# Performance work log

Measured on AMD Instinct MI355X. Metric: run time of the kernel, lower is better.

## Reference

```python
import jax, jax.numpy as jnp
import numpy as np

B, L, D = 4, 2048, 1024
H = 16
HD = D // H


def setup_inputs() -> dict:
    key = jax.random.key(0)
    ks = jax.random.split(key, 6)
    x = jax.random.normal(ks[0], (B, L, D), dtype=jnp.float32)
    # True = masked-out (strict upper triangle -> causal)
    causal_mask = jnp.triu(jnp.ones((L, L), dtype=bool), k=1)
    key_padding_mask = jnp.zeros((B, L), dtype=bool)  # no padding
    lim = 1.0 / np.sqrt(D)
    Wqkv = jax.random.uniform(ks[1], (3 * D, D), minval=-lim, maxval=lim, dtype=jnp.float32)
    bqkv = jax.random.uniform(ks[2], (3 * D,), minval=-lim, maxval=lim, dtype=jnp.float32)
    Wproj = jax.random.uniform(ks[3], (D, D), minval=-lim, maxval=lim, dtype=jnp.float32)
    bproj = jax.random.uniform(ks[4], (D,), minval=-lim, maxval=lim, dtype=jnp.float32)
    return {"x": x, "causal_mask": causal_mask, "key_padding_mask": key_padding_mask,
            "Wqkv": Wqkv, "bqkv": bqkv, "Wproj": Wproj, "bproj": bproj}


def reference(x, causal_mask, key_padding_mask, Wqkv, bqkv, Wproj, bproj):
    b, l, d = x.shape
    scale = (d // H // 1) ** 0  # placeholder; real scale below
    scale = (d // H) ** -0.5
    qkv = x @ Wqkv.T + bqkv                      # [B,L,3D]
    qkv = qkv.reshape(b, l, 3, H, HD).transpose(2, 0, 3, 1, 4)  # [3,B,H,L,HD]
    q, k, v = qkv[0], qkv[1], qkv[2]
    attn = jnp.einsum('bhqd,bhkd->bhqk', q, k) * scale          # [B,H,L,L]
    neg_inf = jnp.float32(-jnp.inf)
    attn = jnp.where(causal_mask[None, None, :, :], neg_inf, attn)
    attn = jnp.where(key_padding_mask[:, None, None, :], neg_inf, attn)
    attn = jax.nn.softmax(attn, axis=-1)
    attn = jnp.nan_to_num(attn, nan=0.0, posinf=0.0, neginf=0.0)
    out = jnp.einsum('bhqk,bhkd->bhqd', attn, v)                # [B,H,L,HD]
    out = out.transpose(0, 2, 1, 3).reshape(b, l, d)
    return out @ Wproj.T + bproj
```

## Files before the change

kernel.cpp:

```cpp
#include <hip/hip_runtime.h>

typedef __bf16 bf16;
typedef __attribute__((ext_vector_type(8))) __bf16 bf16x8;
typedef __attribute__((ext_vector_type(4))) __bf16 bf16x4;
typedef __attribute__((ext_vector_type(4))) float f32x4;
typedef __attribute__((ext_vector_type(4))) short short4v;

#define AS1C(p) ((const __attribute__((address_space(1))) void*)(p))
#define AS3(p)  ((__attribute__((address_space(3))) void*)(p))

static __device__ __forceinline__ f32x4 pv_mfma(bf16x4 a, bf16x4 b, f32x4 c) {
#if __has_builtin(__builtin_amdgcn_mfma_f32_16x16x16bf16_1k)
  return __builtin_amdgcn_mfma_f32_16x16x16bf16_1k(
      __builtin_bit_cast(short4v, a), __builtin_bit_cast(short4v, b), c, 0, 0, 0);
#else
  f32x4 d = c;
  asm("v_mfma_f32_16x16x16_bf16 %0, %1, %2, %0" : "+v"(d) : "v"(a), "v"(b));
  return d;
#endif
}

static __device__ __forceinline__ float fexp2(float x) {
#if __has_builtin(__builtin_amdgcn_exp2f)
  return __builtin_amdgcn_exp2f(x);
#else
  return exp2f(x);
#endif
}
static __device__ __forceinline__ float m3(float a, float b, float c) {
  return fmaxf(fmaxf(a, b), c);
}

__global__ void castk(const float* __restrict__ in, bf16* __restrict__ out, long n) {
  long i = ((long)blockIdx.x * blockDim.x + threadIdx.x) * 4;
  if (i >= n) return;
  f32x4 v = *reinterpret_cast<const f32x4*>(in + i);
  bf16x4 o;
  o[0] = (bf16)v[0]; o[1] = (bf16)v[1]; o[2] = (bf16)v[2]; o[3] = (bf16)v[3];
  *reinterpret_cast<bf16x4*>(out + i) = o;
}

template<int MODE>
__global__ __launch_bounds__(256, 2)
void gemm_bt(const bf16* __restrict__ A, const bf16* __restrict__ BT,
             const float* __restrict__ bias, void* __restrict__ Cout,
             int M, int N, int K) {
  __shared__ bf16 As[128 * 64];
  __shared__ bf16 Bs[128 * 64];
  const int tid = threadIdx.x;
  const int lane = tid & 63;
  const int w = tid >> 6;
  const int wm = w >> 1, wn = w & 1;
  const int row0 = blockIdx.y * 128, col0 = blockIdx.x * 128;

  f32x4 acc[4][4] = {};

  const int srow = tid >> 3;
  const int scb = ((tid & 7) << 4) ^ ((srow & 7) << 4);
  const long aoff = (long)(row0 + srow) * K + (scb >> 1);
  const long boff = (long)(col0 + srow) * K + (scb >> 1);

  for (int k0 = 0; k0 < K; k0 += 64) {
    #pragma unroll
    for (int i = 0; i < 4; ++i) {
      __builtin_amdgcn_global_load_lds(AS1C(A + aoff + (long)i * 32 * K + k0),
                                       AS3((char*)As + i * 4096 + w * 1024), 16, 0, 0);
      __builtin_amdgcn_global_load_lds(AS1C(BT + boff + (long)i * 32 * K + k0),
                                       AS3((char*)Bs + i * 4096 + w * 1024), 16, 0, 0);
    }
    __syncthreads();
    #pragma unroll
    for (int kf = 0; kf < 2; ++kf) {
      bf16x8 af[4], bfr[4];
      #pragma unroll
      for (int m = 0; m < 4; ++m) {
        int r = wm * 64 + m * 16 + (lane & 15);
        int cb = (kf * 64 + ((lane >> 4) << 4)) ^ ((r & 7) << 4);
        af[m] = *reinterpret_cast<const bf16x8*>((const char*)As + r * 128 + cb);
      }
      #pragma unroll
      for (int n = 0; n < 4; ++n) {
        int r = wn * 64 + n * 16 + (lane & 15);
        int cb = (kf * 64 + ((lane >> 4) << 4)) ^ ((r & 7) << 4);
        bfr[n] = *reinterpret_cast<const bf16x8*>((const char*)Bs + r * 128 + cb);
      }
      #pragma unroll
      for (int m = 0; m < 4; ++m)
        #pragma unroll
        for (int n = 0; n < 4; ++n) {
          if constexpr (MODE == 1)
            acc[m][n] = __builtin_amdgcn_mfma_f32_16x16x32_bf16(bfr[n], af[m], acc[m][n], 0, 0, 0);
          else
            acc[m][n] = __builtin_amdgcn_mfma_f32_16x16x32_bf16(af[m], bfr[n], acc[m][n], 0, 0, 0);
        }
    }
    __syncthreads();
  }

  const int g = lane >> 4, q = lane & 15;

  if constexpr (MODE == 0) {
    #pragma unroll
    for (int m = 0; m < 4; ++m)
      #pragma unroll
      for (int n = 0; n < 4; ++n)
        #pragma unroll
        for (int r = 0; r < 4; ++r) {
          int grow = row0 + wm * 64 + m * 16 + g * 4 + r;
          int gcol = col0 + wn * 64 + n * 16 + q;
          reinterpret_cast<float*>(Cout)[(long)grow * N + gcol] = acc[m][n][r] + bias[gcol];
        }
  } else if constexpr (MODE == 1) {
    const int t = (int)blockIdx.x >> 3;
    const int h = (((int)blockIdx.x << 1) | wn) & 15;
    const float qs = (t == 0) ? 0.125f * 1.44269504f : 1.0f;
    bf16* outb = reinterpret_cast<bf16*>(Cout) + (t ? 8388608 : 0);
    #pragma unroll
    for (int n = 0; n < 4; ++n) {
      f32x4 bv = *reinterpret_cast<const f32x4*>(bias + col0 + wn * 64 + n * 16 + g * 4);
      #pragma unroll
      for (int m = 0; m < 4; ++m) {
        int grow = row0 + wm * 64 + m * 16 + q;
        int bb = grow >> 11, ll = grow & 2047;
        bf16x4 o;
        #pragma unroll
        for (int r = 0; r < 4; ++r) o[r] = (bf16)((acc[m][n][r] + bv[r]) * qs);
        *reinterpret_cast<bf16x4*>(outb + ((long)(bb * 16 + h) * 2048 + ll) * 64 + n * 16 + g * 4) = o;
      }
    }
  } else {
    const int h = (((int)blockIdx.x << 1) | wn) & 15;
    bf16* outb = reinterpret_cast<bf16*>(Cout);
    #pragma unroll
    for (int n = 0; n < 4; ++n) {
      float bv = bias[col0 + wn * 64 + n * 16 + q];
      int hd = n * 16 + q;
      #pragma unroll
      for (int m = 0; m < 4; ++m) {
        int grow = row0 + wm * 64 + m * 16 + g * 4;
        int bb = grow >> 11, ll = grow & 2047;
        bf16x4 o;
        #pragma unroll
        for (int r = 0; r < 4; ++r) o[r] = (bf16)(acc[m][n][r] + bv);
        *reinterpret_cast<bf16x4*>(outb + ((long)(bb * 16 + h) * 64 + hd) * 2048 + ll) = o;
      }
    }
  }
}

__global__ __launch_bounds__(512, 8)
void attn_fwd(const bf16* __restrict__ Qg, const bf16* __restrict__ Kg,
              const bf16* __restrict__ VTg, bf16* __restrict__ Og) {
  __shared__ bf16 Ks[2][64 * 64];
  __shared__ bf16 Vs[2][64 * 64];
  const int tid = threadIdx.x, lane = tid & 63, w = tid >> 6;
  const int g = lane >> 4, q = lane & 15;

  const int orig = blockIdx.x;
  const int wgid = (orig & 7) * 128 + (orig >> 3);
  const int bh = wgid >> 4;
  const int qi = 15 - (wgid & 15);
  const int bb = bh >> 4, h = bh & 15;
  const long base = (long)bh * (2048 * 64);
  const int q0 = qi * 128;
  const int qw = q0 + w * 16;
  const int myq = qw + q;

  bf16x8 qf[2];
  qf[0] = *reinterpret_cast<const bf16x8*>(Qg + base + (long)myq * 64 + g * 8);
  qf[1] = *reinterpret_cast<const bf16x8*>(Qg + base + (long)myq * 64 + 32 + g * 8);

  f32x4 accO[4] = {};
  float m = -1e30f, l = 0.f;

  const int srow = tid >> 3;
  const int scb = ((tid & 7) << 4) ^ ((srow & 7) << 4);
  const int nt = 2 * qi + 2;
  const int ntw = (qw >> 6) + 1;

  auto stage = [&](int kt, int buf) {
    __builtin_amdgcn_global_load_lds(
        AS1C(Kg + base + (long)(kt * 64 + srow) * 64 + (scb >> 1)),
        AS3((char*)&Ks[buf][0] + tid * 16), 16, 0, 0);
    __builtin_amdgcn_global_load_lds(
        AS1C(VTg + base + (long)srow * 2048 + kt * 64 + (scb >> 1)),
        AS3((char*)&Vs[buf][0] + tid * 16), 16, 0, 0);
  };

  stage(0, 0);

  for (int kt = 0; kt < nt; ++kt) {
    const int cur = kt & 1;
    __syncthreads();
    if (kt + 1 < nt) stage(kt + 1, cur ^ 1);
    if (kt >= ntw) continue;

    const char* Kb = (const char*)&Ks[cur][0];
    const char* Vb = (const char*)&Vs[cur][0];

    f32x4 sT[4] = {};
    __builtin_amdgcn_s_setprio(1);
    #pragma unroll
    for (int kf = 0; kf < 2; ++kf)
      #pragma unroll
      for (int a = 0; a < 4; ++a) {
        int r = a * 16 + q;
        int cb = (kf * 64 + g * 16) ^ ((r & 7) << 4);
        bf16x8 kb = *reinterpret_cast<const bf16x8*>(Kb + r * 128 + cb);
        sT[a] = __builtin_amdgcn_mfma_f32_16x16x32_bf16(kb, qf[kf], sT[a], 0, 0, 0);
      }
    __builtin_amdgcn_s_setprio(0);

    if (kt == ntw - 1) {
      #pragma unroll
      for (int a = 0; a < 4; ++a)
        #pragma unroll
        for (int r = 0; r < 4; ++r) {
          int kv = kt * 64 + a * 16 + 4 * g + r;
          if (kv > myq) sT[a][r] = -1e30f;
        }
    }

    {
      float t0 = m3(sT[0][0], sT[0][1], sT[0][2]);
      float t1 = m3(sT[0][3], sT[1][0], sT[1][1]);
      float t2 = m3(sT[1][2], sT[1][3], sT[2][0]);
      float t3 = m3(sT[2][1], sT[2][2], sT[2][3]);
      float t4 = m3(sT[3][0], sT[3][1], sT[3][2]);
      float vm = fmaxf(m3(t0, t1, t2), m3(t3, t4, sT[3][3]));
      vm = fmaxf(vm, __shfl_xor(vm, 16));
      vm = fmaxf(vm, __shfl_xor(vm, 32));
      if (__ballot(vm > m + 8.0f)) {
        float mnew = fmaxf(m, vm);
        float fac = fexp2(m - mnew);
        m = mnew;
        #pragma unroll
        for (int b = 0; b < 4; ++b) accO[b] *= fac;
        l *= fac;
      }
    }
    float ps = 0.f;
    bf16x4 pa[4];
    #pragma unroll
    for (int a = 0; a < 4; ++a)
      #pragma unroll
      for (int r = 0; r < 4; ++r) {
        float p = fexp2(sT[a][r] - m);
        ps += p;
        pa[a][r] = (bf16)p;
      }
    ps += __shfl_xor(ps, 16);
    ps += __shfl_xor(ps, 32);
    l += ps;

    __builtin_amdgcn_s_setprio(1);
    #pragma unroll
    for (int a = 0; a < 4; ++a)
      #pragma unroll
      for (int b = 0; b < 4; ++b) {
        int row = b * 16 + q;
        int cb = (a * 32 + g * 8) ^ ((row & 7) << 4);
        bf16x4 vfrag = *reinterpret_cast<const bf16x4*>(Vb + row * 128 + cb);
        accO[b] = pv_mfma(vfrag, pa[a], accO[b]);
      }
    __builtin_amdgcn_s_setprio(0);
  }

  __syncthreads();
  char* ob = (char*)&Ks[0][0] + w * 2048;
  float rl = 1.0f / l;
  #pragma unroll
  for (int b = 0; b < 4; ++b)
    #pragma unroll
    for (int r = 0; r < 4; ++r) {
      int hd = 16 * b + 4 * g + r;
      int cb = (hd * 2) ^ ((q & 7) << 4);
      *reinterpret_cast<bf16*>(ob + q * 128 + cb) = (bf16)(accO[b][r] * rl);
    }
  asm volatile("s_waitcnt lgkmcnt(0)" ::: "memory");
  __builtin_amdgcn_sched_barrier(0);

  const int rr = lane >> 2, cc = lane & 3;
  #pragma unroll
  for (int half = 0; half < 2; ++half) {
    int hd0 = cc * 16 + half * 8;
    int cb = (hd0 * 2) ^ ((rr & 7) << 4);
    bf16x8 vv = *reinterpret_cast<const bf16x8*>(ob + rr * 128 + cb);
    *reinterpret_cast<bf16x8*>(Og + (long)(bb * 2048 + qw + rr) * 1024 + h * 64 + hd0) = vv;
  }
}

extern "C" void kernel_launch(void* const* d_in, const int* in_sizes, int n_in,
                              void* d_out, int out_size, void* d_ws, size_t ws_size,
                              hipStream_t stream) {
  (void)in_sizes; (void)n_in; (void)out_size; (void)ws_size;
  const float* x     = (const float*)d_in[0];
  const float* Wqkv  = (const float*)d_in[3];
  const float* bqkv  = (const float*)d_in[4];
  const float* Wproj = (const float*)d_in[5];
  const float* bproj = (const float*)d_in[6];

  bf16* xb     = (bf16*)d_ws;
  bf16* Wqkvb  = xb + 8388608;
  bf16* Wprojb = Wqkvb + 3145728;
  bf16* Qb     = Wprojb + 1048576;
  bf16* Ob     = Qb + 3 * 8388608;

  castk<<<8192, 256, 0, stream>>>(x, xb, 8388608);
  castk<<<3072, 256, 0, stream>>>(Wqkv, Wqkvb, 3145728);
  castk<<<1024, 256, 0, stream>>>(Wproj, Wprojb, 1048576);

  gemm_bt<1><<<dim3(16, 64), 256, 0, stream>>>(xb, Wqkvb, bqkv, (void*)Qb, 8192, 3072, 1024);
  gemm_bt<2><<<dim3(8, 64), 256, 0, stream>>>(xb, Wqkvb + (long)2048 * 1024, bqkv + 2048,
                                              (void*)(Qb + 16777216), 8192, 3072, 1024);

  attn_fwd<<<dim3(1024), 512, 0, stream>>>(Qb, Qb + 8388608, Qb + 16777216, Ob);

  gemm_bt<0><<<dim3(8, 64), 256, 0, stream>>>(Ob, Wprojb, bproj, d_out, 8192, 1024, 1024);
}
```

Baseline: 215.7 us.

## Load K/V fragments directly from global memory in attention, drop LDS staging

Rewrites the attention kernel so each wave reads its K and V^T MFMA fragments straight from global memory instead of double-buffering 64x64 tiles in shared memory. Blocks shrink from 512 to 256 threads covering 64 queries each, with twice as many blocks, and shared memory is kept only for the output transpose. Removing the per-tile __syncthreads and LDS traffic lets waves run independently and may raise occupancy. The cost is that the four waves in a block each fetch the same K/V tiles, so reuse now depends on L1/L2 and global load latency is exposed without explicit prefetch.

```diff
diff --git a/kernel.cpp b/kernel.cpp
--- a/kernel.cpp
+++ b/kernel.cpp
@@ -148,70 +148,53 @@
   }
 }
 
-__global__ __launch_bounds__(512, 8)
+__global__ __launch_bounds__(256, 5)
 void attn_fwd(const bf16* __restrict__ Qg, const bf16* __restrict__ Kg,
               const bf16* __restrict__ VTg, bf16* __restrict__ Og) {
-  __shared__ bf16 Ks[2][64 * 64];
-  __shared__ bf16 Vs[2][64 * 64];
+  __shared__ bf16 Os[4][16 * 64];
   const int tid = threadIdx.x, lane = tid & 63, w = tid >> 6;
   const int g = lane >> 4, q = lane & 15;
 
   const int orig = blockIdx.x;
-  const int wgid = (orig & 7) * 128 + (orig >> 3);
-  const int bh = wgid >> 4;
-  const int qi = 15 - (wgid & 15);
+  const int wgid = (orig & 7) * 256 + (orig >> 3);
+  const int bh = wgid >> 5;
+  const int qt = 31 - (wgid & 31);
   const int bb = bh >> 4, h = bh & 15;
   const long base = (long)bh * (2048 * 64);
-  const int q0 = qi * 128;
-  const int qw = q0 + w * 16;
+  const int qw = qt * 64 + w * 16;
   const int myq = qw + q;
 
   bf16x8 qf[2];
   qf[0] = *reinterpret_cast<const bf16x8*>(Qg + base + (long)myq * 64 + g * 8);
   qf[1] = *reinterpret_cast<const bf16x8*>(Qg + base + (long)myq * 64 + 32 + g * 8);
 
+  const bf16* kp = Kg + base + q * 64 + g * 8;
+  const bf16* vp = VTg + base + (long)q * 2048 + g * 4;
+
   f32x4 accO[4] = {};
   float m = -1e30f, l = 0.f;
 
-  const int srow = tid >> 3;
-  const int scb = ((tid & 7) << 4) ^ ((srow & 7) << 4);
-  const int nt = 2 * qi + 2;
-  const int ntw = (qw >> 6) + 1;
-
-  auto stage = [&](int kt, int buf) {
-    __builtin_amdgcn_global_load_lds(
-        AS1C(Kg + base + (long)(kt * 64 + srow) * 64 + (scb >> 1)),
-        AS3((char*)&Ks[buf][0] + tid * 16), 16, 0, 0);
-    __builtin_amdgcn_global_load_lds(
-        AS1C(VTg + base + (long)srow * 2048 + kt * 64 + (scb >> 1)),
-        AS3((char*)&Vs[buf][0] + tid * 16), 16, 0, 0);
-  };
-
-  stage(0, 0);
-
-  for (int kt = 0; kt < nt; ++kt) {
-    const int cur = kt & 1;
-    __syncthreads();
-    if (kt + 1 < nt) stage(kt + 1, cur ^ 1);
-    if (kt >= ntw) continue;
-
-    const char* Kb = (const char*)&Ks[cur][0];
-    const char* Vb = (const char*)&Vs[cur][0];
+  for (int kt = 0; kt <= qt; ++kt) {
+    const bf16* kpt = kp + kt * 4096;
+
+    bf16x8 kf0[4], kf1[4];
+    #pragma unroll
+    for (int a = 0; a < 4; ++a) {
+      kf0[a] = *reinterpret_cast<const bf16x8*>(kpt + a * 1024);
+      kf1[a] = *reinterpret_cast<const bf16x8*>(kpt + a * 1024 + 32);
+    }
 
     f32x4 sT[4] = {};
     __builtin_amdgcn_s_setprio(1);
     #pragma unroll
-    for (int kf = 0; kf < 2; ++kf)
-      #pragma unroll
-      for (int a = 0; a < 4; ++a) {
-        int r = a * 16 + q;
-        int cb = (kf * 64 + g * 16) ^ ((r & 7) << 4);
-        bf16x8 kb = *reinterpret_cast<const bf16x8*>(Kb + r * 128 + cb);
-        sT[a] = __builtin_amdgcn_mfma_f32_16x16x32_bf16(kb, qf[kf], sT[a], 0, 0, 0);
-      }
+    for (int a = 0; a < 4; ++a)
+      sT[a] = __builtin_amdgcn_mfma_f32_16x16x32_bf16(kf0[a], qf[0], sT[a], 0, 0, 0);
+    #pragma unroll
+    for (int a = 0; a < 4; ++a)
+      sT[a] = __builtin_amdgcn_mfma_f32_16x16x32_bf16(kf1[a], qf[1], sT[a], 0, 0, 0);
     __builtin_amdgcn_s_setprio(0);
 
-    if (kt == ntw - 1) {
+    if (kt == qt) {
       #pragma unroll
       for (int a = 0; a < 4; ++a)
         #pragma unroll
@@ -253,21 +236,21 @@
     ps += __shfl_xor(ps, 32);
     l += ps;
 
+    const bf16* vpt = vp + kt * 64;
     __builtin_amdgcn_s_setprio(1);
     #pragma unroll
-    for (int a = 0; a < 4; ++a)
-      #pragma unroll
-      for (int b = 0; b < 4; ++b) {
-        int row = b * 16 + q;
-        int cb = (a * 32 + g * 8) ^ ((row & 7) << 4);
-        bf16x4 vfrag = *reinterpret_cast<const bf16x4*>(Vb + row * 128 + cb);
-        accO[b] = pv_mfma(vfrag, pa[a], accO[b]);
-      }
+    for (int b = 0; b < 4; ++b) {
+      const bf16* vb = vpt + (long)b * 32768;
+      #pragma unroll
+      for (int a = 0; a < 4; ++a) {
+        bf16x4 vf = *reinterpret_cast<const bf16x4*>(vb + a * 16);
+        accO[b] = pv_mfma(vf, pa[a], accO[b]);
+      }
+    }
     __builtin_amdgcn_s_setprio(0);
   }
 
-  __syncthreads();
-  char* ob = (char*)&Ks[0][0] + w * 2048;
+  char* ob = (char*)&Os[w][0];
   float rl = 1.0f / l;
   #pragma unroll
   for (int b = 0; b < 4; ++b)
@@ -314,7 +297,7 @@
   gemm_bt<2><<<dim3(8, 64), 256, 0, stream>>>(xb, Wqkvb + (long)2048 * 1024, bqkv + 2048,
                                               (void*)(Qb + 16777216), 8192, 3072, 1024);
 
-  attn_fwd<<<dim3(1024), 512, 0, stream>>>(Qb, Qb + 8388608, Qb + 16777216, Ob);
+  attn_fwd<<<dim3(2048), 256, 0, stream>>>(Qb, Qb + 8388608, Qb + 16777216, Ob);
 
   gemm_bt<0><<<dim3(8, 64), 256, 0, stream>>>(Ob, Wprojb, bproj, d_out, 8192, 1024, 1024);
 }
```

After: 573.0 us. 2.66x slower.
